# Optimization experiments

Hardware: AMD Instinct MI355X
Metric: run time of the kernel (lower is better)

The kernel has to match this reference:

```python
import jax, jax.numpy as jnp
import numpy as np

N_NODES = 50000
N_EDGES = 800000


def _spmm(edge_row, edge_col, edge_w, h):
    # sparse adj @ h via gather + segment-sum: adj[r,c] = edge_w
    msgs = edge_w[:, None] * h[edge_col]          # [E, D] gather
    return jax.ops.segment_sum(msgs, edge_row, num_segments=N_NODES)


def setup_inputs() -> dict:
    key = jax.random.key(0)
    ks = jax.random.split(key, 8)
    x = jax.random.normal(ks[0], (N_NODES, 256), dtype=jnp.float32)
    edge_row = jax.random.randint(ks[1], (N_EDGES,), 0, N_NODES, dtype=jnp.int32)
    edge_col = jax.random.randint(ks[2], (N_EDGES,), 0, N_NODES, dtype=jnp.int32)
    edge_w = jax.random.uniform(ks[3], (N_EDGES,), dtype=jnp.float32)
    W1 = jax.random.normal(ks[4], (256, 128), dtype=jnp.float32) * 0.06
    b1 = jnp.zeros((128,), dtype=jnp.float32)
    W2 = jax.random.normal(ks[5], (128, 32), dtype=jnp.float32) * 0.09
    b2 = jnp.zeros((32,), dtype=jnp.float32)
    return {"x": x, "edge_row": edge_row, "edge_col": edge_col,
            "edge_w": edge_w, "W1": W1, "b1": b1, "W2": W2, "b2": b2}


def reference(x, edge_row, edge_col, edge_w, W1, b1, W2, b2):
    # Layer 1: support = X @ W1 ; out = relu(A @ support + b1)
    # (dropout is identity in eval mode)
    h = jax.nn.relu(_spmm(edge_row, edge_col, edge_w, x @ W1) + b1)
    # Layer 2
    out = jax.nn.relu(_spmm(edge_row, edge_col, edge_w, h @ W2) + b2)
    return out
```

## Files before the change

kernel.cpp:

```cpp
#include <hip/hip_runtime.h>

#define N_NODES 50000
#define N_EDGES 800000
#define D0 256
#define D1 128
#define D2 32
#define CAP 48
#define NB 391
#define BCAP 3072
#define EB 8192
#define SC_BLOCKS 98
#define SW_BLOCKS 4
#define G1_BLOCKS 782
#define RG_BLOCKS 1563
#define NSL 4
#define PL ((size_t)N_NODES * 32)

typedef unsigned short u16;
typedef unsigned int   u32;
typedef unsigned long long u64;
typedef __attribute__((ext_vector_type(8))) short bf16x8;
typedef __attribute__((ext_vector_type(4))) float f32x4;

__device__ inline u32 bf16rne(float f) {
    union { float f; u32 u; } c; c.f = f;
    return (c.u + 0x7FFFu + ((c.u >> 16) & 1u)) >> 16;
}
__device__ inline float bfhi(u32 v) {
    union { u32 u; float f; } c; c.u = v & 0xFFFF0000u; return c.f;
}
__device__ inline float bflo(u32 v) {
    union { u32 u; float f; } c; c.u = v << 16; return c.f;
}

__global__ __launch_bounds__(1024) void scatter_kernel(const int* __restrict__ erow,
                                                       const int* __restrict__ ecol,
                                                       const float* __restrict__ ew,
                                                       u32* __restrict__ bcur,
                                                       u64* __restrict__ ebuf,
                                                       const float* __restrict__ W1,
                                                       u16* __restrict__ Bsw1,
                                                       const float* __restrict__ W2,
                                                       u16* __restrict__ Bsw2) {
    __shared__ u32 hist[NB];
    __shared__ u32 lbase[NB];
    const int tid = threadIdx.x;
    if (blockIdx.x < SC_BLOCKS) {
        if (tid < NB) hist[tid] = 0;
        __syncthreads();
        const int ebase = blockIdx.x * EB;
        #pragma unroll
        for (int k = 0; k < EB / 1024; ++k) {
            const int e = ebase + k * 1024 + tid;
            if (e < N_EDGES) atomicAdd(&hist[erow[e] >> 7], 1u);
        }
        __syncthreads();
        if (tid < NB) {
            const u32 h = hist[tid];
            lbase[tid] = h ? atomicAdd(&bcur[tid], h) : 0u;
            hist[tid] = 0;
        }
        __syncthreads();
        #pragma unroll
        for (int k = 0; k < EB / 1024; ++k) {
            const int e = ebase + k * 1024 + tid;
            if (e < N_EDGES) {
                const int r = erow[e];
                const int c = ecol[e];
                const float w = ew[e];
                const int b = r >> 7;
                const u32 lr = atomicAdd(&hist[b], 1u);
                const u32 pos = lbase[b] + lr;
                if (pos < BCAP)
                    ebuf[(size_t)b * BCAP + pos] =
                        (u64)(u32)c | ((u64)(u32)(r & 127) << 16) | ((u64)bf16rne(w) << 32);
            }
        }
    } else if (blockIdx.x < SC_BLOCKS + SW_BLOCKS) {
        const int id = (blockIdx.x - SC_BLOCKS) * 1024 + tid;
        const int lane = id & 63;
        const int t    = (id >> 6) & 7;
        const int ks   = id >> 9;
        const int n     = t * 16 + (lane & 15);
        const int kbase = ks * 32 + (lane >> 4) * 8;
        u32 v[8];
        #pragma unroll
        for (int j = 0; j < 8; ++j) v[j] = bf16rne(W1[(kbase + j) * D1 + n]);
        uint4 w;
        w.x = v[0] | (v[1] << 16);
        w.y = v[2] | (v[3] << 16);
        w.z = v[4] | (v[5] << 16);
        w.w = v[6] | (v[7] << 16);
        ((uint4*)Bsw1)[id] = w;
    } else if (tid < 512) {
        const int id = tid;
        const int lane = id & 63;
        const int t    = (id >> 6) & 1;
        const int ks   = id >> 7;
        const int n     = t * 16 + (lane & 15);
        const int kbase = ks * 32 + (lane >> 4) * 8;
        u32 v[8];
        #pragma unroll
        for (int j = 0; j < 8; ++j) v[j] = bf16rne(W2[(kbase + j) * D2 + n]);
        uint4 w;
        w.x = v[0] | (v[1] << 16);
        w.y = v[2] | (v[3] << 16);
        w.z = v[4] | (v[5] << 16);
        w.w = v[6] | (v[7] << 16);
        ((uint4*)Bsw2)[id] = w;
    }
}

__global__ __launch_bounds__(256) void gb_kernel(const float* __restrict__ x,
                                                 const u16* __restrict__ Bsw1,
                                                 u16* __restrict__ s1b,
                                                 const u32* __restrict__ bcur,
                                                 const u64* __restrict__ ebuf,
                                                 int* __restrict__ cnt,
                                                 u32* __restrict__ eg) {
    __shared__ u32 seg[128 * CAP];
    __shared__ u32 lcnt[128];
    const int bid = blockIdx.x;
    if (bid < NB) {
        const int b = bid;
        for (int i = threadIdx.x; i < 128; i += 256) lcnt[i] = 0;
        __syncthreads();
        int n = (int)bcur[b];
        if (n > BCAP) n = BCAP;
        const u64* ep = ebuf + (size_t)b * BCAP;
        for (int i = threadIdx.x; i < n; i += 256) {
            const u64 e = ep[i];
            const u32 c  = (u32)(e & 0xFFFFu);
            const u32 lr = (u32)((e >> 16) & 0x7Fu);
            const u32 w  = (u32)(e >> 32);
            const u32 p = atomicAdd(&lcnt[lr], 1u);
            if (p < CAP)
                seg[lr * CAP + p] = c | (w << 16);
        }
        __syncthreads();
        const int rows = min(128, N_NODES - b * 128);
        for (int i = threadIdx.x; i < rows; i += 256)
            cnt[b * 128 + i] = (int)min(lcnt[i], (u32)CAP);
        u32* dst = eg + (size_t)b * 128 * CAP;
        const int nvec = rows * (CAP / 4);
        for (int i = threadIdx.x; i < nvec; i += 256)
            ((uint4*)dst)[i] = ((const uint4*)seg)[i];
    } else {
        const int gb   = bid - NB;
        const int lane = threadIdx.x & 63;
        const int wave = threadIdx.x >> 6;
        const int rowbase = gb * 64 + wave * 16;
        const int m    = lane & 15;
        const int quad = lane >> 4;
        int arow = rowbase + m;
        if (arow >= N_NODES) arow = N_NODES - 1;
        const float* aptr = x + (size_t)arow * D0 + quad * 8;

        f32x4 acc[8];
        #pragma unroll
        for (int t = 0; t < 8; ++t) acc[t] = (f32x4){0.f, 0.f, 0.f, 0.f};

        #pragma unroll
        for (int ks = 0; ks < 8; ++ks) {
            const float4 f0 = *(const float4*)(aptr + ks * 32);
            const float4 f1 = *(const float4*)(aptr + ks * 32 + 4);
            bf16x8 a;
            a[0] = (short)bf16rne(f0.x); a[1] = (short)bf16rne(f0.y);
            a[2] = (short)bf16rne(f0.z); a[3] = (short)bf16rne(f0.w);
            a[4] = (short)bf16rne(f1.x); a[5] = (short)bf16rne(f1.y);
            a[6] = (short)bf16rne(f1.z); a[7] = (short)bf16rne(f1.w);
            const u16* bp = Bsw1 + ((size_t)(ks * 8) * 64 + lane) * 8;
            #pragma unroll
            for (int t = 0; t < 8; ++t) {
                const bf16x8 b = *(const bf16x8*)(bp + (size_t)t * 64 * 8);
                acc[t] = __builtin_amdgcn_mfma_f32_16x16x32_bf16(a, b, acc[t], 0, 0, 0);
            }
        }
        const int orow = rowbase + quad * 4;
        #pragma unroll
        for (int r = 0; r < 4; ++r) {
            const int row = orow + r;
            if (row < N_NODES) {
                #pragma unroll
                for (int t = 0; t < 8; ++t)
                    s1b[(size_t)(t >> 1) * PL + (size_t)row * 32 + (t & 1) * 16 + m] =
                        (u16)bf16rne(acc[t][r]);
            }
        }
    }
}

__global__ __launch_bounds__(256) void spmm1_slice_kernel(const int* __restrict__ cnt,
                                                          const u32* __restrict__ eg,
                                                          const u16* __restrict__ src,
                                                          const float* __restrict__ b1,
                                                          u16* __restrict__ hb) {
    const int tx = threadIdx.x;
    const int s  = blockIdx.x & (NSL - 1);
    const int rg = blockIdx.x >> 2;
    const int row = rg * 32 + threadIdx.y;
    if (row >= N_NODES) return;
    int len = cnt[row];
    if (len > CAP) len = CAP;
    const u32* ep = eg + (size_t)row * CAP;
    const u16* sp = src + (size_t)s * PL;
    float4 a0 = {0.f,0.f,0.f,0.f}, a1 = {0.f,0.f,0.f,0.f};
    float4 a2 = {0.f,0.f,0.f,0.f}, a3 = {0.f,0.f,0.f,0.f};
    int j = 0;
    for (; j + 7 < len; j += 8) {
        const uint4 e4a = *(const uint4*)(ep + j);
        const uint4 e4b = *(const uint4*)(ep + j + 4);
        const uint2 v0 = ((const uint2*)(sp + (size_t)(e4a.x & 0xFFFFu) * 32))[tx];
        const uint2 v1 = ((const uint2*)(sp + (size_t)(e4a.y & 0xFFFFu) * 32))[tx];
        const uint2 v2 = ((const uint2*)(sp + (size_t)(e4a.z & 0xFFFFu) * 32))[tx];
        const uint2 v3 = ((const uint2*)(sp + (size_t)(e4a.w & 0xFFFFu) * 32))[tx];
        const uint2 v4 = ((const uint2*)(sp + (size_t)(e4b.x & 0xFFFFu) * 32))[tx];
        const uint2 v5 = ((const uint2*)(sp + (size_t)(e4b.y & 0xFFFFu) * 32))[tx];
        const uint2 v6 = ((const uint2*)(sp + (size_t)(e4b.z & 0xFFFFu) * 32))[tx];
        const uint2 v7 = ((const uint2*)(sp + (size_t)(e4b.w & 0xFFFFu) * 32))[tx];
        const float w0 = bfhi(e4a.x), w1 = bfhi(e4a.y), w2 = bfhi(e4a.z), w3 = bfhi(e4a.w);
        const float w4 = bfhi(e4b.x), w5 = bfhi(e4b.y), w6 = bfhi(e4b.z), w7 = bfhi(e4b.w);
        a0.x += w0 * bflo(v0.x); a0.y += w0 * bfhi(v0.x);
        a0.z += w0 * bflo(v0.y); a0.w += w0 * bfhi(v0.y);
        a1.x += w1 * bflo(v1.x); a1.y += w1 * bfhi(v1.x);
        a1.z += w1 * bflo(v1.y); a1.w += w1 * bfhi(v1.y);
        a2.x += w2 * bflo(v2.x); a2.y += w2 * bfhi(v2.x);
        a2.z += w2 * bflo(v2.y); a2.w += w2 * bfhi(v2.y);
        a3.x += w3 * bflo(v3.x); a3.y += w3 * bfhi(v3.x);
        a3.z += w3 * bflo(v3.y); a3.w += w3 * bfhi(v3.y);
        a0.x += w4 * bflo(v4.x); a0.y += w4 * bfhi(v4.x);
        a0.z += w4 * bflo(v4.y); a0.w += w4 * bfhi(v4.y);
        a1.x += w5 * bflo(v5.x); a1.y += w5 * bfhi(v5.x);
        a1.z += w5 * bflo(v5.y); a1.w += w5 * bfhi(v5.y);
        a2.x += w6 * bflo(v6.x); a2.y += w6 * bfhi(v6.x);
        a2.z += w6 * bflo(v6.y); a2.w += w6 * bfhi(v6.y);
        a3.x += w7 * bflo(v7.x); a3.y += w7 * bfhi(v7.x);
        a3.z += w7 * bflo(v7.y); a3.w += w7 * bfhi(v7.y);
    }
    for (; j + 3 < len; j += 4) {
        const uint4 e4 = *(const uint4*)(ep + j);
        const uint2 v0 = ((const uint2*)(sp + (size_t)(e4.x & 0xFFFFu) * 32))[tx];
        const uint2 v1 = ((const uint2*)(sp + (size_t)(e4.y & 0xFFFFu) * 32))[tx];
        const uint2 v2 = ((const uint2*)(sp + (size_t)(e4.z & 0xFFFFu) * 32))[tx];
        const uint2 v3 = ((const uint2*)(sp + (size_t)(e4.w & 0xFFFFu) * 32))[tx];
        const float w0 = bfhi(e4.x), w1 = bfhi(e4.y), w2 = bfhi(e4.z), w3 = bfhi(e4.w);
        a0.x += w0 * bflo(v0.x); a0.y += w0 * bfhi(v0.x);
        a0.z += w0 * bflo(v0.y); a0.w += w0 * bfhi(v0.y);
        a1.x += w1 * bflo(v1.x); a1.y += w1 * bfhi(v1.x);
        a1.z += w1 * bflo(v1.y); a1.w += w1 * bfhi(v1.y);
        a2.x += w2 * bflo(v2.x); a2.y += w2 * bfhi(v2.x);
        a2.z += w2 * bflo(v2.y); a2.w += w2 * bfhi(v2.y);
        a3.x += w3 * bflo(v3.x); a3.y += w3 * bfhi(v3.x);
        a3.z += w3 * bflo(v3.y); a3.w += w3 * bfhi(v3.y);
    }
    for (; j < len; ++j) {
        const u32 e0 = ep[j];
        const float w0 = bfhi(e0);
        const uint2 v0 = ((const uint2*)(sp + (size_t)(e0 & 0xFFFFu) * 32))[tx];
        a0.x += w0 * bflo(v0.x); a0.y += w0 * bfhi(v0.x);
        a0.z += w0 * bflo(v0.y); a0.w += w0 * bfhi(v0.y);
    }
    const float4 bv = ((const float4*)(b1 + s * 32))[tx];
    float vx = a0.x + a1.x + a2.x + a3.x + bv.x; vx = vx > 0.f ? vx : 0.f;
    float vy = a0.y + a1.y + a2.y + a3.y + bv.y; vy = vy > 0.f ? vy : 0.f;
    float vz = a0.z + a1.z + a2.z + a3.z + bv.z; vz = vz > 0.f ? vz : 0.f;
    float vw = a0.w + a1.w + a2.w + a3.w + bv.w; vw = vw > 0.f ? vw : 0.f;
    const u64 o = (u64)(bf16rne(vx) | (bf16rne(vy) << 16)) |
                  ((u64)(bf16rne(vz) | (bf16rne(vw) << 16)) << 32);
    __builtin_nontemporal_store(o, (u64*)(hb + (size_t)row * D1 + s * 32) + tx);
}

__global__ __launch_bounds__(256) void gemm2_mfma_kernel(const u16* __restrict__ hb,
                                                         const u16* __restrict__ Bsw2,
                                                         u16* __restrict__ s2b) {
    const int lane = threadIdx.x & 63;
    const int wave = threadIdx.x >> 6;
    const int rowbase = blockIdx.x * 64 + wave * 16;
    const int m    = lane & 15;
    const int quad = lane >> 4;
    int arow = rowbase + m;
    if (arow >= N_NODES) arow = N_NODES - 1;
    const u16* aptr = hb + (size_t)arow * D1 + quad * 8;

    f32x4 acc0 = (f32x4){0.f,0.f,0.f,0.f};
    f32x4 acc1 = (f32x4){0.f,0.f,0.f,0.f};

    #pragma unroll
    for (int ks = 0; ks < 4; ++ks) {
        const bf16x8 a = *(const bf16x8*)(aptr + ks * 32);
        const u16* bp = Bsw2 + ((size_t)(ks * 2) * 64 + lane) * 8;
        const bf16x8 b0 = *(const bf16x8*)(bp);
        const bf16x8 b1 = *(const bf16x8*)(bp + (size_t)64 * 8);
        acc0 = __builtin_amdgcn_mfma_f32_16x16x32_bf16(a, b0, acc0, 0, 0, 0);
        acc1 = __builtin_amdgcn_mfma_f32_16x16x32_bf16(a, b1, acc1, 0, 0, 0);
    }
    const int orow = rowbase + quad * 4;
    #pragma unroll
    for (int r = 0; r < 4; ++r) {
        const int row = orow + r;
        if (row < N_NODES) {
            u16* op = s2b + (size_t)row * D2 + m;
            op[0]  = (u16)bf16rne(acc0[r]);
            op[16] = (u16)bf16rne(acc1[r]);
        }
    }
}

__global__ __launch_bounds__(256) void spmm_csr32_kernel(const int* __restrict__ cnt,
                                                         const u32* __restrict__ eg,
                                                         const u16* __restrict__ src,
                                                         const float* __restrict__ bias,
                                                         float* __restrict__ out) {
    const int lane = threadIdx.x;
    const int row  = blockIdx.x * 16 + threadIdx.y;
    if (row >= N_NODES) return;
    int len = cnt[row];
    if (len > CAP) len = CAP;
    const u32* ep = eg + (size_t)row * CAP;
    float ax0=0.f, ay0=0.f, ax1=0.f, ay1=0.f, ax2=0.f, ay2=0.f, ax3=0.f, ay3=0.f;
    int j = 0;
    for (; j + 7 < len; j += 8) {
        const uint4 e4a = *(const uint4*)(ep + j);
        const uint4 e4b = *(const uint4*)(ep + j + 4);
        const u32 v0 = ((const u32*)(src + (size_t)(e4a.x & 0xFFFFu) * D2))[lane];
        const u32 v1 = ((const u32*)(src + (size_t)(e4a.y & 0xFFFFu) * D2))[lane];
        const u32 v2 = ((const u32*)(src + (size_t)(e4a.z & 0xFFFFu) * D2))[lane];
        const u32 v3 = ((const u32*)(src + (size_t)(e4a.w & 0xFFFFu) * D2))[lane];
        const u32 v4 = ((const u32*)(src + (size_t)(e4b.x & 0xFFFFu) * D2))[lane];
        const u32 v5 = ((const u32*)(src + (size_t)(e4b.y & 0xFFFFu) * D2))[lane];
        const u32 v6 = ((const u32*)(src + (size_t)(e4b.z & 0xFFFFu) * D2))[lane];
        const u32 v7 = ((const u32*)(src + (size_t)(e4b.w & 0xFFFFu) * D2))[lane];
        const float w0 = bfhi(e4a.x), w1 = bfhi(e4a.y), w2 = bfhi(e4a.z), w3 = bfhi(e4a.w);
        const float w4 = bfhi(e4b.x), w5 = bfhi(e4b.y), w6 = bfhi(e4b.z), w7 = bfhi(e4b.w);
        ax0 += w0 * bflo(v0); ay0 += w0 * bfhi(v0);
        ax1 += w1 * bflo(v1); ay1 += w1 * bfhi(v1);
        ax2 += w2 * bflo(v2); ay2 += w2 * bfhi(v2);
        ax3 += w3 * bflo(v3); ay3 += w3 * bfhi(v3);
        ax0 += w4 * bflo(v4); ay0 += w4 * bfhi(v4);
        ax1 += w5 * bflo(v5); ay1 += w5 * bfhi(v5);
        ax2 += w6 * bflo(v6); ay2 += w6 * bfhi(v6);
        ax3 += w7 * bflo(v7); ay3 += w7 * bfhi(v7);
    }
    for (; j + 3 < len; j += 4) {
        const uint4 e4 = *(const uint4*)(ep + j);
        const u32 v0 = ((const u32*)(src + (size_t)(e4.x & 0xFFFFu) * D2))[lane];
        const u32 v1 = ((const u32*)(src + (size_t)(e4.y & 0xFFFFu) * D2))[lane];
        const u32 v2 = ((const u32*)(src + (size_t)(e4.z & 0xFFFFu) * D2))[lane];
        const u32 v3 = ((const u32*)(src + (size_t)(e4.w & 0xFFFFu) * D2))[lane];
        const float w0 = bfhi(e4.x), w1 = bfhi(e4.y), w2 = bfhi(e4.z), w3 = bfhi(e4.w);
        ax0 += w0 * bflo(v0); ay0 += w0 * bfhi(v0);
        ax1 += w1 * bflo(v1); ay1 += w1 * bfhi(v1);
        ax2 += w2 * bflo(v2); ay2 += w2 * bfhi(v2);
        ax3 += w3 * bflo(v3); ay3 += w3 * bfhi(v3);
    }
    for (; j < len; ++j) {
        const u32 e0 = ep[j];
        const u32 v0 = ((const u32*)(src + (size_t)(e0 & 0xFFFFu) * D2))[lane];
        const float w0 = bfhi(e0);
        ax0 += w0 * bflo(v0); ay0 += w0 * bfhi(v0);
    }
    const float2 b2v = ((const float2*)bias)[lane];
    float vx = ax0 + ax1 + ax2 + ax3 + b2v.x; vx = vx > 0.f ? vx : 0.f;
    float vy = ay0 + ay1 + ay2 + ay3 + b2v.y; vy = vy > 0.f ? vy : 0.f;
    union { float2 f; u64 u; } o; o.f = make_float2(vx, vy);
    __builtin_nontemporal_store(o.u, (u64*)(out + (size_t)row * D2) + lane);
}

extern "C" void kernel_launch(void* const* d_in, const int* in_sizes, int n_in,
                              void* d_out, int out_size, void* d_ws, size_t ws_size,
                              hipStream_t stream) {
    const float* x    = (const float*)d_in[0];
    const int*   erow = (const int*)  d_in[1];
    const int*   ecol = (const int*)  d_in[2];
    const float* ew   = (const float*)d_in[3];
    const float* W1   = (const float*)d_in[4];
    const float* b1   = (const float*)d_in[5];
    const float* W2   = (const float*)d_in[6];
    const float* b2   = (const float*)d_in[7];
    float* out = (float*)d_out;

    int* cnt   = (int*)d_ws;
    u32* bcur  = (u32*)(cnt + N_NODES);
    u32* eg    = (u32*)(bcur + 512);
    u16* Bsw1  = (u16*)(eg + (size_t)N_NODES * CAP);
    u16* Bsw2  = Bsw1 + 8 * 8 * 64 * 8;
    u16* s1b   = Bsw2 + 4 * 2 * 64 * 8;
    u16* hb    = s1b + NSL * PL;
    u16* s2b   = hb + (size_t)N_NODES * D1;
    u64* ebuf  = (u64*)(s2b + (size_t)N_NODES * D2);

    hipMemsetAsync(bcur, 0, 512 * sizeof(u32), stream);
    scatter_kernel<<<SC_BLOCKS + SW_BLOCKS + 1, 1024, 0, stream>>>(
        erow, ecol, ew, bcur, ebuf, W1, Bsw1, W2, Bsw2);
    gb_kernel<<<NB + G1_BLOCKS, 256, 0, stream>>>(x, Bsw1, s1b, bcur, ebuf, cnt, eg);
    spmm1_slice_kernel<<<RG_BLOCKS * NSL, dim3(8, 32), 0, stream>>>(cnt, eg, s1b, b1, hb);
    gemm2_mfma_kernel<<<(N_NODES + 63) / 64, 256, 0, stream>>>(hb, Bsw2, s2b);
    spmm_csr32_kernel<<<(N_NODES + 15) / 16, dim3(16, 16), 0, stream>>>(cnt, eg, s2b, b2, out);
}
```

Measured before the change: 183.9 us.

## Co-schedule edge scatter with dense GEMM1 and split weight swizzle and bucketing

The kernel sequence is reorganised. Weight swizzling moves into a tiny front kernel. The edge scatter, now 391 blocks of 256 threads instead of 98 blocks of 1024, runs in the same launch as the X@W1 MFMA GEMM, so the atomic-bound scatter overlaps with the bandwidth-bound GEMM. Per-bucket CSR building moves to its own kernel after that. This adds one launch and more global atomics on bcur (more scatter blocks), in exchange for overlapping the scatter with GEMM1 rather than with bucketing.

```diff
diff --git a/kernel.cpp b/kernel.cpp
--- a/kernel.cpp
+++ b/kernel.cpp
@@ -8,9 +8,8 @@
 #define CAP 48
 #define NB 391
 #define BCAP 3072
-#define EB 8192
-#define SC_BLOCKS 98
-#define SW_BLOCKS 4
+#define EB 2048
+#define SC_BLOCKS 391
 #define G1_BLOCKS 782
 #define RG_BLOCKS 1563
 #define NSL 4
@@ -33,37 +32,77 @@
     union { u32 u; float f; } c; c.u = v << 16; return c.f;
 }
 
-__global__ __launch_bounds__(1024) void scatter_kernel(const int* __restrict__ erow,
-                                                       const int* __restrict__ ecol,
-                                                       const float* __restrict__ ew,
-                                                       u32* __restrict__ bcur,
-                                                       u64* __restrict__ ebuf,
-                                                       const float* __restrict__ W1,
-                                                       u16* __restrict__ Bsw1,
-                                                       const float* __restrict__ W2,
-                                                       u16* __restrict__ Bsw2) {
+__global__ __launch_bounds__(256) void front_kernel(const float* __restrict__ W1,
+                                                    u16* __restrict__ Bsw1,
+                                                    const float* __restrict__ W2,
+                                                    u16* __restrict__ Bsw2) {
+    const int bid = blockIdx.x;
+    if (bid < 16) {
+        const int id = bid * 256 + threadIdx.x;
+        const int lane = id & 63;
+        const int t    = (id >> 6) & 7;
+        const int ks   = id >> 9;
+        const int n     = t * 16 + (lane & 15);
+        const int kbase = ks * 32 + (lane >> 4) * 8;
+        u32 v[8];
+        #pragma unroll
+        for (int j = 0; j < 8; ++j) v[j] = bf16rne(W1[(kbase + j) * D1 + n]);
+        uint4 w;
+        w.x = v[0] | (v[1] << 16);
+        w.y = v[2] | (v[3] << 16);
+        w.z = v[4] | (v[5] << 16);
+        w.w = v[6] | (v[7] << 16);
+        ((uint4*)Bsw1)[id] = w;
+    } else {
+        const int id = (bid - 16) * 256 + threadIdx.x;
+        const int lane = id & 63;
+        const int t    = (id >> 6) & 1;
+        const int ks   = id >> 7;
+        const int n     = t * 16 + (lane & 15);
+        const int kbase = ks * 32 + (lane >> 4) * 8;
+        u32 v[8];
+        #pragma unroll
+        for (int j = 0; j < 8; ++j) v[j] = bf16rne(W2[(kbase + j) * D2 + n]);
+        uint4 w;
+        w.x = v[0] | (v[1] << 16);
+        w.y = v[2] | (v[3] << 16);
+        w.z = v[4] | (v[5] << 16);
+        w.w = v[6] | (v[7] << 16);
+        ((uint4*)Bsw2)[id] = w;
+    }
+}
+
+__global__ __launch_bounds__(256) void mid_kernel(const int* __restrict__ erow,
+                                                  const int* __restrict__ ecol,
+                                                  const float* __restrict__ ew,
+                                                  u32* __restrict__ bcur,
+                                                  u64* __restrict__ ebuf,
+                                                  const float* __restrict__ x,
+                                                  const u16* __restrict__ Bsw1,
+                                                  u16* __restrict__ s1b) {
     __shared__ u32 hist[NB];
     __shared__ u32 lbase[NB];
+    const int bid = blockIdx.x;
     const int tid = threadIdx.x;
-    if (blockIdx.x < SC_BLOCKS) {
-        if (tid < NB) hist[tid] = 0;
+    if (bid < SC_BLOCKS) {
+        for (int i = tid; i < NB; i += 256) hist[i] = 0;
         __syncthreads();
-        const int ebase = blockIdx.x * EB;
-        #pragma unroll
-        for (int k = 0; k < EB / 1024; ++k) {
-            const int e = ebase + k * 1024 + tid;
+        const int ebase = bid * EB;
+        #pragma unroll
+        for (int k = 0; k < EB / 256; ++k) {
+            const int e = ebase + k * 256 + tid;
             if (e < N_EDGES) atomicAdd(&hist[erow[e] >> 7], 1u);
         }
         __syncthreads();
-        if (tid < NB) {
-            const u32 h = hist[tid];
-            lbase[tid] = h ? atomicAdd(&bcur[tid], h) : 0u;
-            hist[tid] = 0;
+        for (int i = tid; i < NB; i += 256) {
+            const u32 h = hist[i];
+            lbase[i] = h ? atomicAdd(&bcur[i], h) : 0u;
+            hist[i] = 0;
         }
         __syncthreads();
         #pragma unroll
-        for (int k = 0; k < EB / 1024; ++k) {
-            const int e = ebase + k * 1024 + tid;
+        for (int k = 0; k < EB / 256; ++k) {
+            const int e = ebase + k * 256 + tid;
             if (e < N_EDGES) {
                 const int r = erow[e];
                 const int c = ecol[e];
@@ -76,79 +115,10 @@
                         (u64)(u32)c | ((u64)(u32)(r & 127) << 16) | ((u64)bf16rne(w) << 32);
             }
         }
-    } else if (blockIdx.x < SC_BLOCKS + SW_BLOCKS) {
-        const int id = (blockIdx.x - SC_BLOCKS) * 1024 + tid;
-        const int lane = id & 63;
-        const int t    = (id >> 6) & 7;
-        const int ks   = id >> 9;
-        const int n     = t * 16 + (lane & 15);
-        const int kbase = ks * 32 + (lane >> 4) * 8;
-        u32 v[8];
-        #pragma unroll
-        for (int j = 0; j < 8; ++j) v[j] = bf16rne(W1[(kbase + j) * D1 + n]);
-        uint4 w;
-        w.x = v[0] | (v[1] << 16);
-        w.y = v[2] | (v[3] << 16);
-        w.z = v[4] | (v[5] << 16);
-        w.w = v[6] | (v[7] << 16);
-        ((uint4*)Bsw1)[id] = w;
-    } else if (tid < 512) {
-        const int id = tid;
-        const int lane = id & 63;
-        const int t    = (id >> 6) & 1;
-        const int ks   = id >> 7;
-        const int n     = t * 16 + (lane & 15);
-        const int kbase = ks * 32 + (lane >> 4) * 8;
-        u32 v[8];
-        #pragma unroll
-        for (int j = 0; j < 8; ++j) v[j] = bf16rne(W2[(kbase + j) * D2 + n]);
-        uint4 w;
-        w.x = v[0] | (v[1] << 16);
-        w.y = v[2] | (v[3] << 16);
-        w.z = v[4] | (v[5] << 16);
-        w.w = v[6] | (v[7] << 16);
-        ((uint4*)Bsw2)[id] = w;
-    }
-}
-
-__global__ __launch_bounds__(256) void gb_kernel(const float* __restrict__ x,
-                                                 const u16* __restrict__ Bsw1,
-                                                 u16* __restrict__ s1b,
-                                                 const u32* __restrict__ bcur,
-                                                 const u64* __restrict__ ebuf,
-                                                 int* __restrict__ cnt,
-                                                 u32* __restrict__ eg) {
-    __shared__ u32 seg[128 * CAP];
-    __shared__ u32 lcnt[128];
-    const int bid = blockIdx.x;
-    if (bid < NB) {
-        const int b = bid;
-        for (int i = threadIdx.x; i < 128; i += 256) lcnt[i] = 0;
-        __syncthreads();
-        int n = (int)bcur[b];
-        if (n > BCAP) n = BCAP;
-        const u64* ep = ebuf + (size_t)b * BCAP;
-        for (int i = threadIdx.x; i < n; i += 256) {
-            const u64 e = ep[i];
-            const u32 c  = (u32)(e & 0xFFFFu);
-            const u32 lr = (u32)((e >> 16) & 0x7Fu);
-            const u32 w  = (u32)(e >> 32);
-            const u32 p = atomicAdd(&lcnt[lr], 1u);
-            if (p < CAP)
-                seg[lr * CAP + p] = c | (w << 16);
-        }
-        __syncthreads();
-        const int rows = min(128, N_NODES - b * 128);
-        for (int i = threadIdx.x; i < rows; i += 256)
-            cnt[b * 128 + i] = (int)min(lcnt[i], (u32)CAP);
-        u32* dst = eg + (size_t)b * 128 * CAP;
-        const int nvec = rows * (CAP / 4);
-        for (int i = threadIdx.x; i < nvec; i += 256)
-            ((uint4*)dst)[i] = ((const uint4*)seg)[i];
     } else {
-        const int gb   = bid - NB;
-        const int lane = threadIdx.x & 63;
-        const int wave = threadIdx.x >> 6;
+        const int gb   = bid - SC_BLOCKS;
+        const int lane = tid & 63;
+        const int wave = tid >> 6;
         const int rowbase = gb * 64 + wave * 16;
         const int m    = lane & 15;
         const int quad = lane >> 4;
@@ -188,6 +158,37 @@
             }
         }
     }
+}
+
+__global__ __launch_bounds__(256) void bucket_kernel(const u32* __restrict__ bcur,
+                                                     const u64* __restrict__ ebuf,
+                                                     int* __restrict__ cnt,
+                                                     u32* __restrict__ eg) {
+    const int b = blockIdx.x;
+    __shared__ u32 seg[128 * CAP];
+    __shared__ u32 lcnt[128];
+    for (int i = threadIdx.x; i < 128; i += 256) lcnt[i] = 0;
+    __syncthreads();
+    int n = (int)bcur[b];
+    if (n > BCAP) n = BCAP;
+    const u64* ep = ebuf + (size_t)b * BCAP;
+    for (int i = threadIdx.x; i < n; i += 256) {
+        const u64 e = ep[i];
+        const u32 c  = (u32)(e & 0xFFFFu);
+        const u32 lr = (u32)((e >> 16) & 0x7Fu);
+        const u32 w  = (u32)(e >> 32);
+        const u32 p = atomicAdd(&lcnt[lr], 1u);
+        if (p < CAP)
+            seg[lr * CAP + p] = c | (w << 16);
+    }
+    __syncthreads();
+    const int rows = min(128, N_NODES - b * 128);
+    for (int i = threadIdx.x; i < rows; i += 256)
+        cnt[b * 128 + i] = (int)min(lcnt[i], (u32)CAP);
+    u32* dst = eg + (size_t)b * 128 * CAP;
+    const int nvec = rows * (CAP / 4);
+    for (int i = threadIdx.x; i < nvec; i += 256)
+        ((uint4*)dst)[i] = ((const uint4*)seg)[i];
 }
 
 __global__ __launch_bounds__(256) void spmm1_slice_kernel(const int* __restrict__ cnt,
@@ -390,9 +391,10 @@
     u64* ebuf  = (u64*)(s2b + (size_t)N_NODES * D2);
 
     hipMemsetAsync(bcur, 0, 512 * sizeof(u32), stream);
-    scatter_kernel<<<SC_BLOCKS + SW_BLOCKS + 1, 1024, 0, stream>>>(
-        erow, ecol, ew, bcur, ebuf, W1, Bsw1, W2, Bsw2);
-    gb_kernel<<<NB + G1_BLOCKS, 256, 0, stream>>>(x, Bsw1, s1b, bcur, ebuf, cnt, eg);
+    front_kernel<<<18, 256, 0, stream>>>(W1, Bsw1, W2, Bsw2);
+    mid_kernel<<<SC_BLOCKS + G1_BLOCKS, 256, 0, stream>>>(
+        erow, ecol, ew, bcur, ebuf, x, Bsw1, s1b);
+    bucket_kernel<<<NB, 256, 0, stream>>>(bcur, ebuf, cnt, eg);
     spmm1_slice_kernel<<<RG_BLOCKS * NSL, dim3(8, 32), 0, stream>>>(cnt, eg, s1b, b1, hb);
     gemm2_mfma_kernel<<<(N_NODES + 63) / 64, 256, 0, stream>>>(hb, Bsw2, s2b);
     spmm_csr32_kernel<<<(N_NODES + 15) / 16, dim3(16, 16), 0, stream>>>(cnt, eg, s2b, b2, out);
```

After: 191.9 us. 1.04x slower.
